# Kernel tuning notes

Measured on AMD Instinct MI355X. Metric: run time of the kernel, lower is better.

The kernel has to match this reference:

```python
import jax, jax.numpy as jnp
import numpy as np

N = 30000      # total nodes across batch
E = 480000     # edges (before self-loops)
B = 48         # graphs in batch
H = 4          # heads
D = 64         # hidden per head
NIN = 8
NOUT = 128
L = 10
SLOPE = 0.2    # GATConv default negative_slope


def setup_inputs() -> dict:
    key = jax.random.key(0)
    ks = jax.random.split(key, 12)
    s = 0.05
    x = jax.random.normal(ks[0], (N, NIN), jnp.float32)
    edge_index = jax.random.randint(ks[1], (2, E), 0, N, dtype=jnp.int32)
    batch = jnp.sort(jax.random.randint(ks[2], (N,), 0, B, dtype=jnp.int32))
    # layer 0 params (input dim NIN)
    W0 = jax.random.normal(ks[3], (NIN, H * D), jnp.float32) * s
    a_src0 = jax.random.normal(ks[4], (H, D), jnp.float32) * s
    a_dst0 = jax.random.normal(ks[5], (H, D), jnp.float32) * s
    b0 = jnp.zeros((H * D,), jnp.float32)
    # layers 1..L-1 (input dim H*D)
    Ws = jax.random.normal(ks[6], (L - 1, H * D, H * D), jnp.float32) * s
    a_srcs = jax.random.normal(ks[7], (L - 1, H, D), jnp.float32) * s
    a_dsts = jax.random.normal(ks[8], (L - 1, H, D), jnp.float32) * s
    bs = jnp.zeros((L - 1, H * D), jnp.float32)
    # readout head: GELU -> Linear(4*H*D -> NOUT)
    head_W = jax.random.normal(ks[9], (4 * H * D, NOUT), jnp.float32) * s
    head_b = jnp.zeros((NOUT,), jnp.float32)
    return dict(x=x, edge_index=edge_index, batch=batch,
                W0=W0, a_src0=a_src0, a_dst0=a_dst0, b0=b0,
                Ws=Ws, a_srcs=a_srcs, a_dsts=a_dsts, bs=bs,
                head_W=head_W, head_b=head_b)


def _gat_layer(x, W, a_src, a_dst, b, src, dst):
    n = x.shape[0]
    h = (x @ W).reshape(n, H, D)                      # [N,H,D]
    alpha_src = jnp.einsum('nhd,hd->nh', h, a_src)    # [N,H]
    alpha_dst = jnp.einsum('nhd,hd->nh', h, a_dst)
    e = jax.nn.leaky_relu(alpha_src[src] + alpha_dst[dst], SLOPE)  # [Etot,H]
    # segment softmax over destination neighborhoods
    m = jax.ops.segment_max(e, dst, num_segments=n)
    e = jnp.exp(e - m[dst])
    z = jax.ops.segment_sum(e, dst, num_segments=n)
    alpha = e / (z[dst] + 1e-16)                      # [Etot,H]
    msg = h[src] * alpha[:, :, None]                  # [Etot,H,D]
    out = jax.ops.segment_sum(msg, dst, num_segments=n)
    return out.reshape(n, H * D) + b


def reference(x, edge_index, batch, W0, a_src0, a_dst0, b0,
              Ws, a_srcs, a_dsts, bs, head_W, head_b):
    # add self loops (GATConv default add_self_loops=True)
    loops = jnp.arange(N, dtype=edge_index.dtype)
    src = jnp.concatenate([edge_index[0], loops])
    dst = jnp.concatenate([edge_index[1], loops])

    h = _gat_layer(x, W0, a_src0, a_dst0, b0, src, dst)
    for i in range(L - 1):
        h = jax.nn.gelu(h, approximate=False)  # dropout = identity (eval)
        h = _gat_layer(h, Ws[i], a_srcs[i], a_dsts[i], bs[i], src, dst)

    # MultiAggregation([min, max, mean, sum]) over graphs
    cnt = jax.ops.segment_sum(jnp.ones((N,), h.dtype), batch, num_segments=B)
    g_sum = jax.ops.segment_sum(h, batch, num_segments=B)
    g_mean = g_sum / jnp.maximum(cnt, 1.0)[:, None]
    g_min = jax.ops.segment_min(h, batch, num_segments=B)
    g_max = jax.ops.segment_max(h, batch, num_segments=B)
    g = jnp.concatenate([g_min, g_max, g_mean, g_sum], axis=-1)  # [B, 4*H*D]

    return jax.nn.gelu(g, approximate=False) @ head_W + head_b   # [B, NOUT]
```

## Files before the change

### kernel.cpp

```cpp
#include <hip/hip_runtime.h>
#include <math.h>

#define NN   30000
#define EE   480000
#define ETOT 510000
#define BB   48
#define HHH  4
#define DDD  64
#define CCH  256
#define NINP 8
#define NOUTP 128
#define NLAY 10
#define SLOPE 0.2f
#define PCHUNK 32

typedef short v8s  __attribute__((ext_vector_type(8)));
typedef float v4f  __attribute__((ext_vector_type(4)));

__device__ __forceinline__ float gelu_f(float x){
    return 0.5f * x * (1.0f + erff(x * 0.70710678118654752f));
}
__device__ __forceinline__ unsigned short f2bf(float f){
    unsigned u = __float_as_uint(f);
    unsigned r = u + 0x7FFF + ((u >> 16) & 1);
    return (unsigned short)(r >> 16);
}
__device__ __forceinline__ float bf2f(unsigned short b){
    return __uint_as_float(((unsigned)b) << 16);
}
__device__ __forceinline__ float lrelu(float e){
    return (e > 0.f) ? e : SLOPE * e;
}
__device__ __forceinline__ float4 up4(uint2 u){
    float4 r;
    r.x = __uint_as_float(u.x << 16);
    r.y = __uint_as_float(u.x & 0xFFFF0000u);
    r.z = __uint_as_float(u.y << 16);
    r.w = __uint_as_float(u.y & 0xFFFF0000u);
    return r;
}

__global__ void count_k(const int* __restrict__ ei, int* __restrict__ cnt){
    int e = blockIdx.x * 256 + threadIdx.x;
    if (e >= ETOT) return;
    int d = (e < EE) ? ei[EE + e] : (e - EE);
    atomicAdd(&cnt[d], 1);
}

__global__ __launch_bounds__(1024) void scan_k(const int* __restrict__ cnt, int* __restrict__ row_ptr){
    const int PER = 30;
    int t = threadIdx.x;
    int base = t * PER;
    int v[PER];
    int sum = 0;
#pragma unroll
    for (int i = 0; i < PER; ++i){
        int x = (base + i < NN) ? cnt[base + i] : 0;
        v[i] = sum;
        sum += x;
    }
    int lane = t & 63, w = t >> 6;
    int inc = sum;
#pragma unroll
    for (int off = 1; off < 64; off <<= 1){
        int u = __shfl_up(inc, off);
        if (lane >= off) inc += u;
    }
    __shared__ int wtot[16], woff[16];
    if (lane == 63) wtot[w] = inc;
    __syncthreads();
    if (t == 0){
        int r = 0;
        for (int i = 0; i < 16; ++i){ woff[i] = r; r += wtot[i]; }
        row_ptr[NN] = r;
    }
    __syncthreads();
    int excl = woff[w] + (inc - sum);
#pragma unroll
    for (int i = 0; i < PER; ++i){
        if (base + i < NN) row_ptr[base + i] = excl + v[i];
    }
}

__global__ void scatter_k(const int* __restrict__ ei, const int* __restrict__ row_ptr,
                          int* __restrict__ cursor, int* __restrict__ csr_src){
    int e = blockIdx.x * 256 + threadIdx.x;
    if (e >= ETOT) return;
    int s, d;
    if (e < EE){ s = ei[e]; d = ei[EE + e]; } else { s = d = e - EE; }
    int pos = row_ptr[d] + atomicAdd(&cursor[d], 1);
    csr_src[pos] = s;
}

__global__ __launch_bounds__(256) void wconv_k(const float* __restrict__ Ws,
                                               unsigned short* __restrict__ WT_hi,
                                               unsigned short* __restrict__ WT_lo){
    __shared__ float tile[32][33];
    int l = blockIdx.x;
    int kt = (blockIdx.y >> 3) * 32;
    int nt = (blockIdx.y & 7) * 32;
    const float* W = Ws + (size_t)l * CCH * CCH;
    unsigned short* th = WT_hi + (size_t)l * CCH * CCH;
    unsigned short* tl = WT_lo + (size_t)l * CCH * CCH;
    int tx = threadIdx.x & 31, ty = threadIdx.x >> 5;
#pragma unroll
    for (int r = ty; r < 32; r += 8)
        tile[r][tx] = W[(size_t)(kt + r) * CCH + nt + tx];
    __syncthreads();
#pragma unroll
    for (int r = ty; r < 32; r += 8){
        float w = tile[tx][r];
        unsigned short h = f2bf(w);
        size_t o = (size_t)(nt + r) * CCH + kt + tx;
        th[o] = h;
        tl[o] = f2bf(w - bf2f(h));
    }
}

__global__ __launch_bounds__(256) void waconv_k(const float* __restrict__ Ws,
                                                const float* __restrict__ a_srcs,
                                                const float* __restrict__ a_dsts,
                                                unsigned short* __restrict__ wa_hi,
                                                unsigned short* __restrict__ wa_lo){
    int l = blockIdx.x;
    int j = blockIdx.y;
    int k = threadIdx.x;
    const float* W = Ws + (size_t)l * CCH * CCH;
    const float* av = (j < 4) ? (a_srcs + (size_t)l * CCH + j * DDD)
                              : (a_dsts + (size_t)l * CCH + (j - 4) * DDD);
    int cb = (j & 3) * DDD;
    float s = 0.f;
    const float4* wp = (const float4*)(W + (size_t)k * CCH + cb);
    const float4* ap = (const float4*)av;
#pragma unroll
    for (int d = 0; d < DDD / 4; ++d){
        float4 wv = wp[d], avv = ap[d];
        s += wv.x * avv.x + wv.y * avv.y + wv.z * avv.z + wv.w * avv.w;
    }
    unsigned short hb = f2bf(s);
    wa_hi[((size_t)l * 16 + j) * CCH + k] = hb;
    wa_lo[((size_t)l * 16 + j) * CCH + k] = f2bf(s - bf2f(hb));
    if (j >= 4){
        wa_hi[((size_t)l * 16 + j + 4) * CCH + k] = 0;
        wa_lo[((size_t)l * 16 + j + 4) * CCH + k] = 0;
        wa_hi[((size_t)l * 16 + j + 8) * CCH + k] = 0;
        wa_lo[((size_t)l * 16 + j + 8) * CCH + k] = 0;
    }
}

__global__ __launch_bounds__(256) void l0_fused(const float* __restrict__ x,
                                                const float* __restrict__ W0,
                                                const float* __restrict__ a_src,
                                                const float* __restrict__ a_dst,
                                                unsigned short* __restrict__ hout,
                                                float* __restrict__ asb,
                                                float* __restrict__ adb){
    __shared__ float xs[NINP];
    int n = blockIdx.x;
    int c = threadIdx.x;
    if (c < NINP) xs[c] = x[n * NINP + c];
    __syncthreads();
    float acc = 0.f;
#pragma unroll
    for (int k = 0; k < NINP; ++k) acc += xs[k] * W0[k * CCH + c];
    hout[(size_t)n * CCH + c] = f2bf(acc);
    int hh = c >> 6, lane = c & 63;
    float s1 = acc * a_src[hh * DDD + lane];
    float s2 = acc * a_dst[hh * DDD + lane];
#pragma unroll
    for (int off = 32; off; off >>= 1){
        s1 += __shfl_xor(s1, off);
        s2 += __shfl_xor(s2, off);
    }
    if (lane == 0){
        asb[(size_t)n * HHH + hh] = s1;
        adb[(size_t)n * HHH + hh] = s2;
    }
}

__global__ __launch_bounds__(256) void gemm_mfma(const float* __restrict__ A,
                                                 const unsigned short* __restrict__ Bhi,
                                                 const unsigned short* __restrict__ Blo,
                                                 const unsigned short* __restrict__ WAhi,
                                                 const unsigned short* __restrict__ WAlo,
                                                 unsigned short* __restrict__ C,
                                                 float* __restrict__ asb,
                                                 float* __restrict__ adb){
    int tid  = threadIdx.x;
    int lane = tid & 63, wave = tid >> 6;
    int wr = wave >> 1, wc = wave & 1;
    int rowBase = blockIdx.y * 128 + wr * 64;
    int colBase = blockIdx.x * 128 + wc * 64;
    int fr = lane & 15;
    int kg = lane >> 4;
    bool doAlpha = (blockIdx.x == 0) && (wc == 0);

    v4f acc[4][4];
#pragma unroll
    for (int mi = 0; mi < 4; ++mi)
#pragma unroll
        for (int ni = 0; ni < 4; ++ni) acc[mi][ni] = (v4f){0.f, 0.f, 0.f, 0.f};
    v4f acca[4];
#pragma unroll
    for (int mi = 0; mi < 4; ++mi) acca[mi] = (v4f){0.f, 0.f, 0.f, 0.f};

    const float* aptr[4];
#pragma unroll
    for (int mi = 0; mi < 4; ++mi){
        int r = rowBase + mi * 16 + fr;
        if (r >= NN) r = NN - 1;
        aptr[mi] = A + (size_t)r * CCH + kg * 8;
    }
    const unsigned short* bhp[4];
    const unsigned short* blp[4];
#pragma unroll
    for (int ni = 0; ni < 4; ++ni){
        int c = colBase + ni * 16 + fr;
        bhp[ni] = Bhi + (size_t)c * CCH + kg * 8;
        blp[ni] = Blo + (size_t)c * CCH + kg * 8;
    }
    const unsigned short* wahp = WAhi + (size_t)fr * CCH + kg * 8;
    const unsigned short* walp = WAlo + (size_t)fr * CCH + kg * 8;

    for (int kc = 0; kc < CCH; kc += 32){
        v8s ah[4], al[4], bh[4], bl[4];
#pragma unroll
        for (int mi = 0; mi < 4; ++mi){
            float4 v0 = *(const float4*)(aptr[mi] + kc);
            float4 v1 = *(const float4*)(aptr[mi] + kc + 4);
            float f[8] = {v0.x, v0.y, v0.z, v0.w, v1.x, v1.y, v1.z, v1.w};
            v8s hi, lo;
#pragma unroll
            for (int j = 0; j < 8; ++j){
                float g = gelu_f(f[j]);
                unsigned short hb = f2bf(g);
                hi[j] = (short)hb;
                lo[j] = (short)f2bf(g - bf2f(hb));
            }
            ah[mi] = hi; al[mi] = lo;
        }
#pragma unroll
        for (int ni = 0; ni < 4; ++ni){
            bh[ni] = *(const v8s*)(bhp[ni] + kc);
            bl[ni] = *(const v8s*)(blp[ni] + kc);
        }
#pragma unroll
        for (int mi = 0; mi < 4; ++mi)
#pragma unroll
            for (int ni = 0; ni < 4; ++ni){
                acc[mi][ni] = __builtin_amdgcn_mfma_f32_16x16x32_bf16(ah[mi], bh[ni], acc[mi][ni], 0, 0, 0);
                acc[mi][ni] = __builtin_amdgcn_mfma_f32_16x16x32_bf16(al[mi], bh[ni], acc[mi][ni], 0, 0, 0);
                acc[mi][ni] = __builtin_amdgcn_mfma_f32_16x16x32_bf16(ah[mi], bl[ni], acc[mi][ni], 0, 0, 0);
            }
        if (doAlpha){
            v8s wh = *(const v8s*)(wahp + kc);
            v8s wl = *(const v8s*)(walp + kc);
#pragma unroll
            for (int mi = 0; mi < 4; ++mi){
                acca[mi] = __builtin_amdgcn_mfma_f32_16x16x32_bf16(ah[mi], wh, acca[mi], 0, 0, 0);
                acca[mi] = __builtin_amdgcn_mfma_f32_16x16x32_bf16(al[mi], wh, acca[mi], 0, 0, 0);
                acca[mi] = __builtin_amdgcn_mfma_f32_16x16x32_bf16(ah[mi], wl, acca[mi], 0, 0, 0);
            }
        }
    }

#pragma unroll
    for (int mi = 0; mi < 4; ++mi)
#pragma unroll
        for (int j = 0; j < 4; ++j){
            int r = rowBase + mi * 16 + kg * 4 + j;
            if (r < NN){
#pragma unroll
                for (int ni = 0; ni < 4; ++ni)
                    C[(size_t)r * CCH + colBase + ni * 16 + fr] = f2bf(acc[mi][ni][j]);
            }
        }
    if (doAlpha){
#pragma unroll
        for (int mi = 0; mi < 4; ++mi)
#pragma unroll
            for (int j = 0; j < 4; ++j){
                int r = rowBase + mi * 16 + kg * 4 + j;
                if (r < NN){
                    float val = acca[mi][j];
                    if (fr < 4)      asb[(size_t)r * HHH + fr]       = val;
                    else if (fr < 8) adb[(size_t)r * HHH + (fr - 4)] = val;
                }
            }
    }
}

#define LOADG8(gg, U0, U1, U2, U3, A0, A1, A2, A3)                     \
    { int _b = (gg) << 3;                                              \
      int _e0 = _b + half, _e1 = _b + 2 + half;                        \
      int _e2 = _b + 4 + half, _e3 = _b + 6 + half;                    \
      int _i0 = ix_w[_e0], _i1 = ix_w[_e1];                            \
      int _i2 = ix_w[_e2], _i3 = ix_w[_e3];                            \
      A0 = al_w[_e0 * HHH + hc8];                                      \
      A1 = al_w[_e1 * HHH + hc8];                                      \
      A2 = al_w[_e2 * HHH + hc8];                                      \
      A3 = al_w[_e3 * HHH + hc8];                                      \
      U0 = *(const uint4*)(h + (size_t)_i0 * CCH + coff8);             \
      U1 = *(const uint4*)(h + (size_t)_i1 * CCH + coff8);             \
      U2 = *(const uint4*)(h + (size_t)_i2 * CCH + coff8);             \
      U3 = *(const uint4*)(h + (size_t)_i3 * CCH + coff8); }

#define CONSUME8(U0, U1, U2, U3, A0, A1, A2, A3)                       \
    { float4 _l0 = up4(make_uint2(U0.x, U0.y)), _h0 = up4(make_uint2(U0.z, U0.w)); \
      float4 _l1 = up4(make_uint2(U1.x, U1.y)), _h1 = up4(make_uint2(U1.z, U1.w)); \
      float4 _l2 = up4(make_uint2(U2.x, U2.y)), _h2 = up4(make_uint2(U2.z, U2.w)); \
      float4 _l3 = up4(make_uint2(U3.x, U3.y)), _h3 = up4(make_uint2(U3.z, U3.w)); \
      accLo.x += _l0.x * A0 + _l1.x * A1 + _l2.x * A2 + _l3.x * A3;    \
      accLo.y += _l0.y * A0 + _l1.y * A1 + _l2.y * A2 + _l3.y * A3;    \
      accLo.z += _l0.z * A0 + _l1.z * A1 + _l2.z * A2 + _l3.z * A3;    \
      accLo.w += _l0.w * A0 + _l1.w * A1 + _l2.w * A2 + _l3.w * A3;    \
      accHi.x += _h0.x * A0 + _h1.x * A1 + _h2.x * A2 + _h3.x * A3;    \
      accHi.y += _h0.y * A0 + _h1.y * A1 + _h2.y * A2 + _h3.y * A3;    \
      accHi.z += _h0.z * A0 + _h1.z * A1 + _h2.z * A2 + _h3.z * A3;    \
      accHi.w += _h0.w * A0 + _h1.w * A1 + _h2.w * A2 + _h3.w * A3; }

__global__ __launch_bounds__(256) void agg_k(const unsigned short* __restrict__ h,
                                             const float* __restrict__ asrc,
                                             const float* __restrict__ adst,
                                             const float* __restrict__ bias,
                                             const int* __restrict__ row_ptr,
                                             const int* __restrict__ csr_src,
                                             float* __restrict__ out){
    __shared__ float s_al[4][64 * HHH];
    __shared__ int   s_ix[4][64];

    int wave = threadIdx.x >> 6, lane = threadIdx.x & 63;
    int n = blockIdx.x * 4 + wave;
    int row0 = row_ptr[n];
    int deg  = row_ptr[n + 1] - row0;
    float4 ad = *(const float4*)(adst + (size_t)n * HHH);
    float* al_w = s_al[wave];
    int*   ix_w = s_ix[wave];

    if (deg <= 64){
        int k = lane;
        int s = 0;
        float e0 = -INFINITY, e1 = -INFINITY, e2 = -INFINITY, e3 = -INFINITY;
        if (k < deg){
            s = csr_src[row0 + k];
            float4 as = *(const float4*)(asrc + (size_t)s * HHH);
            e0 = lrelu(as.x + ad.x); e1 = lrelu(as.y + ad.y);
            e2 = lrelu(as.z + ad.z); e3 = lrelu(as.w + ad.w);
        }
        float m0 = e0, m1 = e1, m2 = e2, m3 = e3;
#pragma unroll
        for (int off = 32; off; off >>= 1){
            m0 = fmaxf(m0, __shfl_xor(m0, off));
            m1 = fmaxf(m1, __shfl_xor(m1, off));
            m2 = fmaxf(m2, __shfl_xor(m2, off));
            m3 = fmaxf(m3, __shfl_xor(m3, off));
        }
        float x0 = 0.f, x1 = 0.f, x2 = 0.f, x3 = 0.f;
        if (k < deg){
            x0 = __expf(e0 - m0); x1 = __expf(e1 - m1);
            x2 = __expf(e2 - m2); x3 = __expf(e3 - m3);
        }
        float z0 = x0, z1 = x1, z2 = x2, z3 = x3;
#pragma unroll
        for (int off = 32; off; off >>= 1){
            z0 += __shfl_xor(z0, off);
            z1 += __shfl_xor(z1, off);
            z2 += __shfl_xor(z2, off);
            z3 += __shfl_xor(z3, off);
        }
        if (k < deg){
            float4 alv;
            alv.x = x0 / (z0 + 1e-16f);
            alv.y = x1 / (z1 + 1e-16f);
            alv.z = x2 / (z2 + 1e-16f);
            alv.w = x3 / (z3 + 1e-16f);
            ix_w[k] = s;
            *(float4*)&al_w[k * HHH] = alv;
        }
        int half  = lane >> 5;
        int l32   = lane & 31;
        int coff8 = l32 << 3;
        int hc8   = l32 >> 3;
        float4 accLo = make_float4(0.f, 0.f, 0.f, 0.f);
        float4 accHi = make_float4(0.f, 0.f, 0.f, 0.f);

        int ng = deg >> 3;
        uint4 uA0, uA1, uA2, uA3, uB0, uB1, uB2, uB3;
        float aA0, aA1, aA2, aA3, aB0, aB1, aB2, aB3;
        if (ng > 0) LOADG8(0, uA0, uA1, uA2, uA3, aA0, aA1, aA2, aA3);
        if (ng > 1) LOADG8(1, uB0, uB1, uB2, uB3, aB0, aB1, aB2, aB3);
        for (int g = 0; g < ng; g += 2){
            if (g + 2 < ng) {
                CONSUME8(uA0, uA1, uA2, uA3, aA0, aA1, aA2, aA3);
                LOADG8(g + 2, uA0, uA1, uA2, uA3, aA0, aA1, aA2, aA3);
            } else {
                CONSUME8(uA0, uA1, uA2, uA3, aA0, aA1, aA2, aA3);
            }
            if (g + 1 < ng){
                if (g + 3 < ng) {
                    CONSUME8(uB0, uB1, uB2, uB3, aB0, aB1, aB2, aB3);
                    LOADG8(g + 3, uB0, uB1, uB2, uB3, aB0, aB1, aB2, aB3);
                } else {
                    CONSUME8(uB0, uB1, uB2, uB3, aB0, aB1, aB2, aB3);
                }
            }
        }
        for (int kk = ng << 3; kk < deg; kk += 2){
            int e = kk + half;
            if (e < deg){
                int i0 = ix_w[e];
                float a0 = al_w[e * HHH + hc8];
                uint4 u = *(const uint4*)(h + (size_t)i0 * CCH + coff8);
                float4 lo = up4(make_uint2(u.x, u.y)), hi = up4(make_uint2(u.z, u.w));
                accLo.x += lo.x * a0; accLo.y += lo.y * a0;
                accLo.z += lo.z * a0; accLo.w += lo.w * a0;
                accHi.x += hi.x * a0; accHi.y += hi.y * a0;
                accHi.z += hi.z * a0; accHi.w += hi.w * a0;
            }
        }
        accLo.x += __shfl_xor(accLo.x, 32); accLo.y += __shfl_xor(accLo.y, 32);
        accLo.z += __shfl_xor(accLo.z, 32); accLo.w += __shfl_xor(accLo.w, 32);
        accHi.x += __shfl_xor(accHi.x, 32); accHi.y += __shfl_xor(accHi.y, 32);
        accHi.z += __shfl_xor(accHi.z, 32); accHi.w += __shfl_xor(accHi.w, 32);
        if (half == 0){
            float4 b0v = *(const float4*)(bias + coff8);
            float4 b1v = *(const float4*)(bias + coff8 + 4);
            accLo.x += b0v.x; accLo.y += b0v.y; accLo.z += b0v.z; accLo.w += b0v.w;
            accHi.x += b1v.x; accHi.y += b1v.y; accHi.z += b1v.z; accHi.w += b1v.w;
            *(float4*)(out + (size_t)n * CCH + coff8)     = accLo;
            *(float4*)(out + (size_t)n * CCH + coff8 + 4) = accHi;
        }
        return;
    }

    int coff = lane << 2;
    int hc   = lane >> 4;
    float4 acc = make_float4(0.f, 0.f, 0.f, 0.f);
    float m0 = -INFINITY, m1 = -INFINITY, m2 = -INFINITY, m3 = -INFINITY;
    float z0 = 0.f, z1 = 0.f, z2 = 0.f, z3 = 0.f;
    for (int c0 = 0; c0 < deg; c0 += 64){
        int k = c0 + lane;
        float e0 = -INFINITY, e1 = -INFINITY, e2 = -INFINITY, e3 = -INFINITY;
        if (k < deg){
            int s = csr_src[row0 + k];
            float4 as = *(const float4*)(asrc + (size_t)s * HHH);
            e0 = lrelu(as.x + ad.x); e1 = lrelu(as.y + ad.y);
            e2 = lrelu(as.z + ad.z); e3 = lrelu(as.w + ad.w);
        }
        float c0m = e0, c1m = e1, c2m = e2, c3m = e3;
#pragma unroll
        for (int off = 32; off; off >>= 1){
            c0m = fmaxf(c0m, __shfl_xor(c0m, off));
            c1m = fmaxf(c1m, __shfl_xor(c1m, off));
            c2m = fmaxf(c2m, __shfl_xor(c2m, off));
            c3m = fmaxf(c3m, __shfl_xor(c3m, off));
        }
        float n0 = fmaxf(m0, c0m), n1 = fmaxf(m1, c1m);
        float n2 = fmaxf(m2, c2m), n3 = fmaxf(m3, c3m);
        float x0 = 0.f, x1 = 0.f, x2 = 0.f, x3 = 0.f;
        if (k < deg){
            x0 = __expf(e0 - n0); x1 = __expf(e1 - n1);
            x2 = __expf(e2 - n2); x3 = __expf(e3 - n3);
        }
        float s0 = x0, s1 = x1, s2 = x2, s3 = x3;
#pragma unroll
        for (int off = 32; off; off >>= 1){
            s0 += __shfl_xor(s0, off);
            s1 += __shfl_xor(s1, off);
            s2 += __shfl_xor(s2, off);
            s3 += __shfl_xor(s3, off);
        }
        z0 = z0 * ((m0 == -INFINITY) ? 0.f : __expf(m0 - n0)) + s0;
        z1 = z1 * ((m1 == -INFINITY) ? 0.f : __expf(m1 - n1)) + s1;
        z2 = z2 * ((m2 == -INFINITY) ? 0.f : __expf(m2 - n2)) + s2;
        z3 = z3 * ((m3 == -INFINITY) ? 0.f : __expf(m3 - n3)) + s3;
        m0 = n0; m1 = n1; m2 = n2; m3 = n3;
    }
    float iz0 = 1.f / (z0 + 1e-16f), iz1 = 1.f / (z1 + 1e-16f);
    float iz2 = 1.f / (z2 + 1e-16f), iz3 = 1.f / (z3 + 1e-16f);
    for (int c0 = 0; c0 < deg; c0 += 64){
        int k = c0 + lane;
        if (k < deg){
            int s = csr_src[row0 + k];
            float4 as = *(const float4*)(asrc + (size_t)s * HHH);
            float4 alv;
            alv.x = __expf(lrelu(as.x + ad.x) - m0) * iz0;
            alv.y = __expf(lrelu(as.y + ad.y) - m1) * iz1;
            alv.z = __expf(lrelu(as.z + ad.z) - m2) * iz2;
            alv.w = __expf(lrelu(as.w + ad.w) - m3) * iz3;
            ix_w[lane] = s;
            *(float4*)&al_w[lane * HHH] = alv;
        }
        int cnt = deg - c0; if (cnt > 64) cnt = 64;
        for (int j = 0; j < cnt; ++j){
            int i0 = ix_w[j];
            float a0 = al_w[j * HHH + hc];
            float4 v0 = up4(*(const uint2*)(h + (size_t)i0 * CCH + coff));
            acc.x += v0.x * a0; acc.y += v0.y * a0; acc.z += v0.z * a0; acc.w += v0.w * a0;
        }
    }
    float4 bv = *(const float4*)(bias + coff);
    acc.x += bv.x; acc.y += bv.y; acc.z += bv.z; acc.w += bv.w;
    *(float4*)(out + (size_t)n * CCH + coff) = acc;
}

__global__ void gptr_k(const int* __restrict__ batch, int* __restrict__ gptr){
    int i = blockIdx.x * 256 + threadIdx.x;
    if (i >= NN) return;
    int bi = batch[i];
    int bp = (i == 0) ? -1 : batch[i - 1];
    for (int g = bp + 1; g <= bi; ++g) gptr[g] = i;
    if (i == NN - 1){
        for (int g = bi + 1; g <= BB; ++g) gptr[g] = NN;
    }
}

__global__ __launch_bounds__(256) void pool1_k(const float* __restrict__ h,
                                               const int* __restrict__ gptr,
                                               float* __restrict__ part){
    const int S1 = BB * PCHUNK * CCH;
    int b = blockIdx.x, j = blockIdx.y, c = threadIdx.x;
    int s = gptr[b], e = gptr[b + 1];
    int len = e - s;
    int per = (len + PCHUNK - 1) / PCHUNK;
    int r0 = s + j * per;
    int r1 = r0 + per; if (r1 > e) r1 = e;
    float mn = INFINITY, mx = -INFINITY, sm = 0.f;
    int n = r0;
    for (; n + 4 <= r1; n += 4){
        float v0 = h[(size_t)(n + 0) * CCH + c];
        float v1 = h[(size_t)(n + 1) * CCH + c];
        float v2 = h[(size_t)(n + 2) * CCH + c];
        float v3 = h[(size_t)(n + 3) * CCH + c];
        mn = fminf(mn, fminf(fminf(v0, v1), fminf(v2, v3)));
        mx = fmaxf(mx, fmaxf(fmaxf(v0, v1), fmaxf(v2, v3)));
        sm += (v0 + v1) + (v2 + v3);
    }
    for (; n < r1; ++n){
        float v = h[(size_t)n * CCH + c];
        mn = fminf(mn, v); mx = fmaxf(mx, v); sm += v;
    }
    size_t o = ((size_t)b * PCHUNK + j) * CCH + c;
    part[o] = mn; part[S1 + o] = mx; part[2 * (size_t)S1 + o] = sm;
}

__global__ __launch_bounds__(256) void pool2_k(const float* __restrict__ part,
                                               const int* __restrict__ gptr,
                                               float* __restrict__ gbuf){
    const int S1 = BB * PCHUNK * CCH;
    int b = blockIdx.x, c = threadIdx.x;
    float mn = INFINITY, mx = -INFINITY, sm = 0.f;
#pragma unroll
    for (int j = 0; j < PCHUNK; ++j){
        size_t o = ((size_t)b * PCHUNK + j) * CCH + c;
        mn = fminf(mn, part[o]);
        mx = fmaxf(mx, part[S1 + o]);
        sm += part[2 * (size_t)S1 + o];
    }
    int cnt = gptr[b + 1] - gptr[b];
    float mean = sm / fmaxf((float)cnt, 1.0f);
    if (cnt == 0){ mn = 0.f; mx = 0.f; }
    gbuf[b * 4 * CCH + 0 * CCH + c] = mn;
    gbuf[b * 4 * CCH + 1 * CCH + c] = mx;
    gbuf[b * 4 * CCH + 2 * CCH + c] = mean;
    gbuf[b * 4 * CCH + 3 * CCH + c] = sm;
}

__global__ __launch_bounds__(128) void head_k(const float* __restrict__ gbuf,
                                              const float* __restrict__ head_W,
                                              const float* __restrict__ head_b,
                                              float* __restrict__ out){
    __shared__ float gs[4 * CCH];
    int b = blockIdx.x;
    int o = threadIdx.x;
    for (int k = o; k < 4 * CCH; k += 128) gs[k] = gelu_f(gbuf[b * 4 * CCH + k]);
    __syncthreads();
    float acc = head_b[o];
    for (int k = 0; k < 4 * CCH; ++k) acc += gs[k] * head_W[k * NOUTP + o];
    out[b * NOUTP + o] = acc;
}

extern "C" void kernel_launch(void* const* d_in, const int* in_sizes, int n_in,
                              void* d_out, int out_size, void* d_ws, size_t ws_size,
                              hipStream_t stream){
    const float* x        = (const float*)d_in[0];
    const int*   ei       = (const int*)  d_in[1];
    const int*   batch    = (const int*)  d_in[2];
    const float* W0       = (const float*)d_in[3];
    const float* a_src0   = (const float*)d_in[4];
    const float* a_dst0   = (const float*)d_in[5];
    const float* b0       = (const float*)d_in[6];
    const float* Ws       = (const float*)d_in[7];
    const float* a_srcs   = (const float*)d_in[8];
    const float* a_dsts   = (const float*)d_in[9];
    const float* bs       = (const float*)d_in[10];
    const float* head_W   = (const float*)d_in[11];
    const float* head_b   = (const float*)d_in[12];
    float* out = (float*)d_out;

    char* p = (char*)d_ws;
    float* buf0 = (float*)p;                   p += (size_t)NN * CCH * 4;
    unsigned short* buf1 = (unsigned short*)p; p += (size_t)NN * CCH * 2;
    float* asb  = (float*)p;                   p += (size_t)NN * HHH * 4;
    float* adb  = (float*)p;                   p += (size_t)NN * HHH * 4;
    int* row_ptr = (int*)p;                    p += 120016;
    int* cnt     = (int*)p;                    p += (size_t)NN * 4;
    int* csr_src = (int*)p;                    p += (size_t)ETOT * 4;
    float* gbuf  = (float*)p;                  p += (size_t)BB * 4 * CCH * 4;
    int* gptr    = (int*)p;                    p += 208;
    unsigned short* wthi = (unsigned short*)p; p += (size_t)(NLAY - 1) * CCH * CCH * 2;
    unsigned short* wtlo = (unsigned short*)p; p += (size_t)(NLAY - 1) * CCH * CCH * 2;
    unsigned short* wahi = (unsigned short*)p; p += (size_t)(NLAY - 1) * 16 * CCH * 2;
    unsigned short* walo = (unsigned short*)p; p += (size_t)(NLAY - 1) * 16 * CCH * 2;
    float* pscr = (float*)p;                   p += (size_t)3 * BB * PCHUNK * CCH * 4;

    hipMemsetAsync(cnt, 0, (size_t)NN * 4, stream);
    count_k<<<(ETOT + 255) / 256, 256, 0, stream>>>(ei, cnt);
    scan_k<<<1, 1024, 0, stream>>>(cnt, row_ptr);
    hipMemsetAsync(cnt, 0, (size_t)NN * 4, stream);
    scatter_k<<<(ETOT + 255) / 256, 256, 0, stream>>>(ei, row_ptr, cnt, csr_src);
    gptr_k<<<(NN + 255) / 256, 256, 0, stream>>>(batch, gptr);
    wconv_k<<<dim3(NLAY - 1, 64), 256, 0, stream>>>(Ws, wthi, wtlo);
    waconv_k<<<dim3(NLAY - 1, 8), 256, 0, stream>>>(Ws, a_srcs, a_dsts, wahi, walo);

    l0_fused<<<NN, 256, 0, stream>>>(x, W0, a_src0, a_dst0, buf1, asb, adb);
    agg_k<<<NN / 4, 256, 0, stream>>>(buf1, asb, adb, b0, row_ptr, csr_src, buf0);

    dim3 ggrid(2, (NN + 127) / 128);
    for (int l = 1; l < NLAY; ++l){
        const unsigned short* whl = wthi + (size_t)(l - 1) * CCH * CCH;
        const unsigned short* wll = wtlo + (size_t)(l - 1) * CCH * CCH;
        const unsigned short* wal_h = wahi + (size_t)(l - 1) * 16 * CCH;
        const unsigned short* wal_l = walo + (size_t)(l - 1) * 16 * CCH;
        const float* bl  = bs + (size_t)(l - 1) * CCH;
        gemm_mfma<<<ggrid, 256, 0, stream>>>(buf0, whl, wll, wal_h, wal_l, buf1, asb, adb);
        agg_k<<<NN / 4, 256, 0, stream>>>(buf1, asb, adb, bl, row_ptr, csr_src, buf0);
    }

    dim3 pgrid(BB, PCHUNK);
    pool1_k<<<pgrid, 256, 0, stream>>>(buf0, gptr, pscr);
    pool2_k<<<BB, 256, 0, stream>>>(pscr, gptr, gbuf);
    head_k<<<BB, 128, 0, stream>>>(gbuf, head_W, head_b, out);
}
```

Measured before the change: 1.121 ms.

## Fuse GELU into aggregation epilogue and store bf16 activations for GEMM

```diff
diff --git a/kernel.cpp b/kernel.cpp
--- a/kernel.cpp
+++ b/kernel.cpp
@@ -30,6 +30,9 @@
 }
 __device__ __forceinline__ float lrelu(float e){
     return (e > 0.f) ? e : SLOPE * e;
+}
+__device__ __forceinline__ unsigned pack2(float a, float b){
+    return (unsigned)f2bf(a) | ((unsigned)f2bf(b) << 16);
 }
 __device__ __forceinline__ float4 up4(uint2 u){
     float4 r;
@@ -178,7 +181,7 @@
     }
 }
 
-__global__ __launch_bounds__(256) void gemm_mfma(const float* __restrict__ A,
+__global__ __launch_bounds__(256) void gemm_mfma(const unsigned short* __restrict__ A,
                                                  const unsigned short* __restrict__ Bhi,
                                                  const unsigned short* __restrict__ Blo,
                                                  const unsigned short* __restrict__ WAhi,
@@ -204,7 +207,7 @@
 #pragma unroll
     for (int mi = 0; mi < 4; ++mi) acca[mi] = (v4f){0.f, 0.f, 0.f, 0.f};
 
-    const float* aptr[4];
+    const unsigned short* aptr[4];
 #pragma unroll
     for (int mi = 0; mi < 4; ++mi){
         int r = rowBase + mi * 16 + fr;
@@ -223,22 +226,9 @@
     const unsigned short* walp = WAlo + (size_t)fr * CCH + kg * 8;
 
     for (int kc = 0; kc < CCH; kc += 32){
-        v8s ah[4], al[4], bh[4], bl[4];
-#pragma unroll
-        for (int mi = 0; mi < 4; ++mi){
-            float4 v0 = *(const float4*)(aptr[mi] + kc);
-            float4 v1 = *(const float4*)(aptr[mi] + kc + 4);
-            float f[8] = {v0.x, v0.y, v0.z, v0.w, v1.x, v1.y, v1.z, v1.w};
-            v8s hi, lo;
-#pragma unroll
-            for (int j = 0; j < 8; ++j){
-                float g = gelu_f(f[j]);
-                unsigned short hb = f2bf(g);
-                hi[j] = (short)hb;
-                lo[j] = (short)f2bf(g - bf2f(hb));
-            }
-            ah[mi] = hi; al[mi] = lo;
-        }
+        v8s a[4], bh[4], bl[4];
+#pragma unroll
+        for (int mi = 0; mi < 4; ++mi) a[mi] = *(const v8s*)(aptr[mi] + kc);
 #pragma unroll
         for (int ni = 0; ni < 4; ++ni){
             bh[ni] = *(const v8s*)(bhp[ni] + kc);
@@ -248,18 +238,16 @@
         for (int mi = 0; mi < 4; ++mi)
 #pragma unroll
             for (int ni = 0; ni < 4; ++ni){
-                acc[mi][ni] = __builtin_amdgcn_mfma_f32_16x16x32_bf16(ah[mi], bh[ni], acc[mi][ni], 0, 0, 0);
-                acc[mi][ni] = __builtin_amdgcn_mfma_f32_16x16x32_bf16(al[mi], bh[ni], acc[mi][ni], 0, 0, 0);
-                acc[mi][ni] = __builtin_amdgcn_mfma_f32_16x16x32_bf16(ah[mi], bl[ni], acc[mi][ni], 0, 0, 0);
+                acc[mi][ni] = __builtin_amdgcn_mfma_f32_16x16x32_bf16(a[mi], bh[ni], acc[mi][ni], 0, 0, 0);
+                acc[mi][ni] = __builtin_amdgcn_mfma_f32_16x16x32_bf16(a[mi], bl[ni], acc[mi][ni], 0, 0, 0);
             }
         if (doAlpha){
             v8s wh = *(const v8s*)(wahp + kc);
             v8s wl = *(const v8s*)(walp + kc);
 #pragma unroll
             for (int mi = 0; mi < 4; ++mi){
-                acca[mi] = __builtin_amdgcn_mfma_f32_16x16x32_bf16(ah[mi], wh, acca[mi], 0, 0, 0);
-                acca[mi] = __builtin_amdgcn_mfma_f32_16x16x32_bf16(al[mi], wh, acca[mi], 0, 0, 0);
-                acca[mi] = __builtin_amdgcn_mfma_f32_16x16x32_bf16(ah[mi], wl, acca[mi], 0, 0, 0);
+                acca[mi] = __builtin_amdgcn_mfma_f32_16x16x32_bf16(a[mi], wh, acca[mi], 0, 0, 0);
+                acca[mi] = __builtin_amdgcn_mfma_f32_16x16x32_bf16(a[mi], wl, acca[mi], 0, 0, 0);
             }
         }
     }
@@ -325,7 +313,9 @@
                                              const float* __restrict__ bias,
                                              const int* __restrict__ row_ptr,
                                              const int* __restrict__ csr_src,
-                                             float* __restrict__ out){
+                                             unsigned short* __restrict__ outg,
+                                             float* __restrict__ outf,
+                                             int mode){
     __shared__ float s_al[4][64 * HHH];
     __shared__ int   s_ix[4][64];
 
@@ -427,8 +417,17 @@
             float4 b1v = *(const float4*)(bias + coff8 + 4);
             accLo.x += b0v.x; accLo.y += b0v.y; accLo.z += b0v.z; accLo.w += b0v.w;
             accHi.x += b1v.x; accHi.y += b1v.y; accHi.z += b1v.z; accHi.w += b1v.w;
-            *(float4*)(out + (size_t)n * CCH + coff8)     = accLo;
-            *(float4*)(out + (size_t)n * CCH + coff8 + 4) = accHi;
+            if (mode == 0){
+                uint4 o;
+                o.x = pack2(gelu_f(accLo.x), gelu_f(accLo.y));
+                o.y = pack2(gelu_f(accLo.z), gelu_f(accLo.w));
+                o.z = pack2(gelu_f(accHi.x), gelu_f(accHi.y));
+                o.w = pack2(gelu_f(accHi.z), gelu_f(accHi.w));
+                *(uint4*)(outg + (size_t)n * CCH + coff8) = o;
+            } else {
+                *(float4*)(outf + (size_t)n * CCH + coff8)     = accLo;
+                *(float4*)(outf + (size_t)n * CCH + coff8 + 4) = accHi;
+            }
         }
         return;
     }
@@ -501,7 +500,14 @@
     }
     float4 bv = *(const float4*)(bias + coff);
     acc.x += bv.x; acc.y += bv.y; acc.z += bv.z; acc.w += bv.w;
-    *(float4*)(out + (size_t)n * CCH + coff) = acc;
+    if (mode == 0){
+        uint2 o;
+        o.x = pack2(gelu_f(acc.x), gelu_f(acc.y));
+        o.y = pack2(gelu_f(acc.z), gelu_f(acc.w));
+        *(uint2*)(outg + (size_t)n * CCH + coff) = o;
+    } else {
+        *(float4*)(outf + (size_t)n * CCH + coff) = acc;
+    }
 }
 
 __global__ void gptr_k(const int* __restrict__ batch, int* __restrict__ gptr){
@@ -599,8 +605,9 @@
     float* out = (float*)d_out;
 
     char* p = (char*)d_ws;
-    float* buf0 = (float*)p;                   p += (size_t)NN * CCH * 4;
-    unsigned short* buf1 = (unsigned short*)p; p += (size_t)NN * CCH * 2;
+    float* buf0f = (float*)p;                   p += (size_t)NN * CCH * 4;
+    unsigned short* buf0g = (unsigned short*)p; p += (size_t)NN * CCH * 2;
+    unsigned short* buf1  = (unsigned short*)p; p += (size_t)NN * CCH * 2;
     float* asb  = (float*)p;                   p += (size_t)NN * HHH * 4;
     float* adb  = (float*)p;                   p += (size_t)NN * HHH * 4;
     int* row_ptr = (int*)p;                    p += 120016;
@@ -624,7 +631,8 @@
     waconv_k<<<dim3(NLAY - 1, 8), 256, 0, stream>>>(Ws, a_srcs, a_dsts, wahi, walo);
 
     l0_fused<<<NN, 256, 0, stream>>>(x, W0, a_src0, a_dst0, buf1, asb, adb);
-    agg_k<<<NN / 4, 256, 0, stream>>>(buf1, asb, adb, b0, row_ptr, csr_src, buf0);
+    agg_k<<<NN / 4, 256, 0, stream>>>(buf1, asb, adb, b0, row_ptr, csr_src,
+                                      buf0g, buf0f, 0);
 
     dim3 ggrid(2, (NN + 127) / 128);
     for (int l = 1; l < NLAY; ++l){
@@ -633,12 +641,13 @@
         const unsigned short* wal_h = wahi + (size_t)(l - 1) * 16 * CCH;
         const unsigned short* wal_l = walo + (size_t)(l - 1) * 16 * CCH;
         const float* bl  = bs + (size_t)(l - 1) * CCH;
-        gemm_mfma<<<ggrid, 256, 0, stream>>>(buf0, whl, wll, wal_h, wal_l, buf1, asb, adb);
-        agg_k<<<NN / 4, 256, 0, stream>>>(buf1, asb, adb, bl, row_ptr, csr_src, buf0);
+        gemm_mfma<<<ggrid, 256, 0, stream>>>(buf0g, whl, wll, wal_h, wal_l, buf1, asb, adb);
+        agg_k<<<NN / 4, 256, 0, stream>>>(buf1, asb, adb, bl, row_ptr, csr_src,
+                                          buf0g, buf0f, (l == NLAY - 1) ? 1 : 0);
     }
 
     dim3 pgrid(BB, PCHUNK);
-    pool1_k<<<pgrid, 256, 0, stream>>>(buf0, gptr, pscr);
+    pool1_k<<<pgrid, 256, 0, stream>>>(buf0f, gptr, pscr);
     pool2_k<<<BB, 256, 0, stream>>>(pscr, gptr, gbuf);
     head_k<<<BB, 128, 0, stream>>>(gbuf, head_W, head_b, out);
 }
```

Result: faster. 979.6 us (-12.6%).
